# Optimization experiments

Hardware: AMD Instinct MI355X
Metric: run time of the kernel (lower is better)

Reference implementation:

```python
import jax, jax.numpy as jnp
import numpy as np

N = 20000      # nodes
E = 640000     # edges (before self-loops)
NFEAT = 512
NHID = 128
HEADS = 2
NOUT = 64
K = 100
ALPHA = 0.2          # LeakyReLU negative slope
CLUSTER_TEMP = 5.0


def gat_layer(x, W, a_src, a_dst, b, src, dst, n, heads, out_c, neg_slope):
    """PyG-style GATConv (eval mode, self-loops already in src/dst).
    W: [heads*out_c, in_c], a_src/a_dst: [heads, out_c], b: [heads*out_c]."""
    h = (x @ W.T).reshape(n, heads, out_c)               # [N,H,C]
    alpha_src = (h * a_src[None]).sum(-1)                # [N,H]
    alpha_dst = (h * a_dst[None]).sum(-1)                # [N,H]
    e = alpha_src[src] + alpha_dst[dst]                  # [E',H]
    e = jnp.where(e > 0, e, neg_slope * e)               # LeakyReLU
    # segment softmax over incoming edges of each dst node
    m = jax.ops.segment_max(e, dst, num_segments=n)
    ex = jnp.exp(e - m[dst])
    s = jax.ops.segment_sum(ex, dst, num_segments=n)
    a = ex / (s[dst] + 1e-16)                            # [E',H]
    out = jax.ops.segment_sum(h[src] * a[:, :, None], dst, num_segments=n)
    return out.reshape(n, heads * out_c) + b


def cluster_iter(data_n, mu, num_iter, cluster_temp):
    """Soft k-means on row-normalized data. data_n: [N,D], mu: [K,D]."""
    def body(mu, _):
        dist = data_n @ mu.T                              # [N,K]
        r = jax.nn.softmax(cluster_temp * dist, axis=1)
        cluster_r = r.sum(axis=0)                         # [K]
        cluster_mean = r.T @ data_n                       # [K,D]
        return cluster_mean / cluster_r[:, None], None
    mu, _ = jax.lax.scan(body, mu, None, length=num_iter)
    dist = data_n @ mu.T
    r = jax.nn.softmax(cluster_temp * dist, axis=1)
    return mu, r, dist


def setup_inputs() -> dict:
    key = jax.random.key(0)
    ks = jax.random.split(key, 12)
    x = jax.random.normal(ks[0], (N, NFEAT), dtype=jnp.float32)
    edge_index = jax.random.randint(ks[1], (2, E), 0, N, dtype=jnp.int32)
    # GATConv layer 1 params
    W1 = jax.random.normal(ks[2], (HEADS * NHID, NFEAT), dtype=jnp.float32) * 0.05
    a_src1 = jax.random.normal(ks[3], (HEADS, NHID), dtype=jnp.float32) * 0.1
    a_dst1 = jax.random.normal(ks[4], (HEADS, NHID), dtype=jnp.float32) * 0.1
    b1 = jnp.zeros((HEADS * NHID,), dtype=jnp.float32)
    # GATConv layer 2 params (heads=1)
    W2 = jax.random.normal(ks[5], (NOUT, HEADS * NHID), dtype=jnp.float32) * 0.05
    a_src2 = jax.random.normal(ks[6], (1, NOUT), dtype=jnp.float32) * 0.1
    a_dst2 = jax.random.normal(ks[7], (1, NOUT), dtype=jnp.float32) * 0.1
    b2 = jnp.zeros((NOUT,), dtype=jnp.float32)
    # cluster init (self.init = torch.rand(K, nout))
    mu0 = jax.random.uniform(ks[8], (K, NOUT), dtype=jnp.float32)
    return {"x": x, "W1": W1, "a_src1": a_src1, "a_dst1": a_dst1, "b1": b1,
            "W2": W2, "a_src2": a_src2, "a_dst2": a_dst2, "b2": b2,
            "mu0": mu0, "edge_index": edge_index, "num_iter": 10}


def reference(x, W1, a_src1, a_dst1, b1, W2, a_src2, a_dst2, b2, mu0,
              edge_index, num_iter):
    loops = jnp.arange(N, dtype=edge_index.dtype)
    src = jnp.concatenate([edge_index[0], loops])
    dst = jnp.concatenate([edge_index[1], loops])
    h = jax.nn.elu(gat_layer(x, W1, a_src1, a_dst1, b1, src, dst,
                             N, HEADS, NHID, ALPHA))
    embeds = gat_layer(h, W2, a_src2, a_dst2, b2, src, dst,
                       N, 1, NOUT, ALPHA) + 1e-6
    data_n = embeds / jnp.linalg.norm(embeds, axis=1, keepdims=True)
    mu_init, _, _ = cluster_iter(data_n, mu0, num_iter, CLUSTER_TEMP)
    mu, r, dist = cluster_iter(data_n, jax.lax.stop_gradient(mu_init), 1,
                               CLUSTER_TEMP)
    return mu, r, embeds, dist
```

## Files before the change

### kernel.cpp

```cpp
#include <hip/hip_runtime.h>
#include <math.h>

#define Nn 20000
#define Ee 640000
#define ETOT 660000
#define NF 512
#define C1 256
#define C2 64
#define KC 100
#define TEMP 5.0f
#define NSLOPE 0.2f
#define NPART 250
#define CHB 80

__device__ __forceinline__ float wredSum(float v) {
#pragma unroll
  for (int off = 32; off > 0; off >>= 1) v += __shfl_xor(v, off, 64);
  return v;
}
__device__ __forceinline__ float wredMax(float v) {
#pragma unroll
  for (int off = 32; off > 0; off >>= 1) v = fmaxf(v, __shfl_xor(v, off, 64));
  return v;
}
__device__ __forceinline__ float bredSum(float v, volatile float* red) {
  v = wredSum(v);
  __syncthreads();
  if ((threadIdx.x & 63) == 0) red[threadIdx.x >> 6] = v;
  __syncthreads();
  return red[0] + red[1] + red[2] + red[3];
}
__device__ __forceinline__ float bredMax(float v, volatile float* red) {
  v = wredMax(v);
  __syncthreads();
  if ((threadIdx.x & 63) == 0) red[threadIdx.x >> 6] = v;
  __syncthreads();
  return fmaxf(fmaxf(red[0], red[1]), fmaxf(red[2], red[3]));
}

__global__ void hist_kernel(const int* __restrict__ ei, int* __restrict__ deg) {
  int e = blockIdx.x * 256 + threadIdx.x;
  if (e >= ETOT) return;
  int dst = e < Ee ? ei[Ee + e] : e - Ee;
  atomicAdd(&deg[dst], 1);
}

__global__ __launch_bounds__(1024) void scan2_kernel(const int* __restrict__ deg,
    int* __restrict__ rowp, int* __restrict__ curs) {
  __shared__ int wsum[16];
  __shared__ int wpre[16];
  int t = threadIdx.x;
  int lane = t & 63, w = t >> 6;
  int loc[20];
  int tot = 0;
  int base = t * 20;
  if (t < 1000) {
#pragma unroll
    for (int i = 0; i < 20; i++) { tot += deg[base + i]; loc[i] = tot; }
  }
  int s = tot;
#pragma unroll
  for (int off = 1; off < 64; off <<= 1) {
    int u = __shfl_up(s, off, 64);
    if (lane >= off) s += u;
  }
  if (lane == 63) wsum[w] = s;
  __syncthreads();
  if (t == 0) {
    int c = 0;
#pragma unroll
    for (int i = 0; i < 16; i++) { c += wsum[i]; wpre[i] = c; }
    rowp[0] = 0;
  }
  __syncthreads();
  int p = (w > 0 ? wpre[w - 1] : 0) + s - tot;
  if (t < 1000) {
    int prev = 0;
#pragma unroll
    for (int i = 0; i < 20; i++) {
      rowp[base + i + 1] = p + loc[i];
      curs[base + i] = p + prev;
      prev = loc[i];
    }
  }
}

__global__ void scatter_kernel(const int* __restrict__ ei, int* __restrict__ curs,
                               int* __restrict__ esort) {
  int e = blockIdx.x * 256 + threadIdx.x;
  if (e >= ETOT) return;
  int dst = e < Ee ? ei[Ee + e] : e - Ee;
  int pos = atomicAdd(&curs[dst], 1);
  esort[pos] = e;
}

__global__ __launch_bounds__(256) void gemm128(const float* __restrict__ A,
    const float* __restrict__ B, float* __restrict__ C, int M, int N, int K) {
  __shared__ __align__(16) float As[16][132];
  __shared__ __align__(16) float Bs[16][132];
  int tid = threadIdx.x;
  int bm = blockIdx.x << 7, bn = blockIdx.y << 7;
  int tx = tid & 15, ty = tid >> 4;
  int r0 = tid >> 2;
  int c0 = (tid & 3) << 2;
  float acc[2][2][4][4] = {};
  for (int k0 = 0; k0 < K; k0 += 16) {
    float4 a0 = make_float4(0.f, 0.f, 0.f, 0.f), a1 = a0;
    int am0 = bm + r0, am1 = bm + 64 + r0;
    if (am0 < M) a0 = *(const float4*)(A + (size_t)am0 * K + k0 + c0);
    if (am1 < M) a1 = *(const float4*)(A + (size_t)am1 * K + k0 + c0);
    float4 b0 = *(const float4*)(B + (size_t)(bn + r0) * K + k0 + c0);
    float4 b1 = *(const float4*)(B + (size_t)(bn + 64 + r0) * K + k0 + c0);
    __syncthreads();
    As[c0 + 0][r0] = a0.x; As[c0 + 1][r0] = a0.y; As[c0 + 2][r0] = a0.z; As[c0 + 3][r0] = a0.w;
    As[c0 + 0][64 + r0] = a1.x; As[c0 + 1][64 + r0] = a1.y; As[c0 + 2][64 + r0] = a1.z; As[c0 + 3][64 + r0] = a1.w;
    Bs[c0 + 0][r0] = b0.x; Bs[c0 + 1][r0] = b0.y; Bs[c0 + 2][r0] = b0.z; Bs[c0 + 3][r0] = b0.w;
    Bs[c0 + 0][64 + r0] = b1.x; Bs[c0 + 1][64 + r0] = b1.y; Bs[c0 + 2][64 + r0] = b1.z; Bs[c0 + 3][64 + r0] = b1.w;
    __syncthreads();
#pragma unroll
    for (int k = 0; k < 16; k++) {
      float4 av0 = *(const float4*)&As[k][ty << 2];
      float4 av1 = *(const float4*)&As[k][64 + (ty << 2)];
      float4 bv0 = *(const float4*)&Bs[k][tx << 2];
      float4 bv1 = *(const float4*)&Bs[k][64 + (tx << 2)];
      float aa[2][4] = {{av0.x, av0.y, av0.z, av0.w}, {av1.x, av1.y, av1.z, av1.w}};
      float bb[2][4] = {{bv0.x, bv0.y, bv0.z, bv0.w}, {bv1.x, bv1.y, bv1.z, bv1.w}};
#pragma unroll
      for (int im = 0; im < 2; im++)
#pragma unroll
        for (int i = 0; i < 4; i++)
#pragma unroll
          for (int jn = 0; jn < 2; jn++)
#pragma unroll
            for (int j = 0; j < 4; j++)
              acc[im][jn][i][j] += aa[im][i] * bb[jn][j];
    }
  }
#pragma unroll
  for (int im = 0; im < 2; im++)
#pragma unroll
    for (int i = 0; i < 4; i++) {
      int row = bm + (im << 6) + (ty << 2) + i;
      if (row < M) {
#pragma unroll
        for (int jn = 0; jn < 2; jn++) {
          float4 v = make_float4(acc[im][jn][i][0], acc[im][jn][i][1],
                                 acc[im][jn][i][2], acc[im][jn][i][3]);
          *(float4*)(C + (size_t)row * N + bn + (jn << 6) + (tx << 2)) = v;
        }
      }
    }
}

__global__ __launch_bounds__(256) void gemm_nt(const float* __restrict__ A,
    const float* __restrict__ B, float* __restrict__ C, int M, int N, int K) {
  __shared__ __align__(16) float As[16][68];
  __shared__ __align__(16) float Bs[16][68];
  int tid = threadIdx.x;
  int bm = blockIdx.x << 6, bn = blockIdx.y << 6;
  int lr = tid >> 2;
  int lc = (tid & 3) << 2;
  int tx = tid & 15, ty = tid >> 4;
  float acc[4][4] = {};
  for (int k0 = 0; k0 < K; k0 += 16) {
    int am = bm + lr;
    float4 av = make_float4(0.f, 0.f, 0.f, 0.f);
    if (am < M) av = *(const float4*)(A + (size_t)am * K + k0 + lc);
    float4 bv = *(const float4*)(B + (size_t)(bn + lr) * K + k0 + lc);
    __syncthreads();
    As[lc + 0][lr] = av.x; As[lc + 1][lr] = av.y; As[lc + 2][lr] = av.z; As[lc + 3][lr] = av.w;
    Bs[lc + 0][lr] = bv.x; Bs[lc + 1][lr] = bv.y; Bs[lc + 2][lr] = bv.z; Bs[lc + 3][lr] = bv.w;
    __syncthreads();
#pragma unroll
    for (int k = 0; k < 16; k++) {
      float4 a = *(const float4*)&As[k][ty << 2];
      float4 b = *(const float4*)&Bs[k][tx << 2];
      float aa[4] = {a.x, a.y, a.z, a.w};
      float bb[4] = {b.x, b.y, b.z, b.w};
#pragma unroll
      for (int i = 0; i < 4; i++)
#pragma unroll
        for (int j = 0; j < 4; j++) acc[i][j] += aa[i] * bb[j];
    }
  }
#pragma unroll
  for (int i = 0; i < 4; i++) {
    int row = bm + (ty << 2) + i;
    if (row < M) {
#pragma unroll
      for (int j = 0; j < 4; j++)
        C[(size_t)row * N + bn + (tx << 2) + j] = acc[i][j];
    }
  }
}

__global__ __launch_bounds__(256) void alpha1_kernel(const float* __restrict__ h,
    const float* __restrict__ a_src, const float* __restrict__ a_dst,
    float* __restrict__ asn, float* __restrict__ adn) {
  int l = threadIdx.x & 63;
  int n = (blockIdx.x << 2) + (threadIdx.x >> 6);
  if (n >= Nn) return;
  const float* hr = h + (size_t)n * C1;
  float h0 = hr[l], h1v = hr[64 + l], h2v = hr[128 + l], h3v = hr[192 + l];
  float ps0 = h0 * a_src[l] + h1v * a_src[64 + l];
  float pd0 = h0 * a_dst[l] + h1v * a_dst[64 + l];
  float ps1 = h2v * a_src[128 + l] + h3v * a_src[192 + l];
  float pd1 = h2v * a_dst[128 + l] + h3v * a_dst[192 + l];
  ps0 = wredSum(ps0); pd0 = wredSum(pd0); ps1 = wredSum(ps1); pd1 = wredSum(pd1);
  if (l == 0) {
    asn[2 * n] = ps0; asn[2 * n + 1] = ps1;
    adn[2 * n] = pd0; adn[2 * n + 1] = pd1;
  }
}

__global__ __launch_bounds__(256) void alpha2_kernel(const float* __restrict__ h,
    const float* __restrict__ a_src, const float* __restrict__ a_dst,
    float* __restrict__ asn, float* __restrict__ adn) {
  int l = threadIdx.x & 63;
  int n = (blockIdx.x << 2) + (threadIdx.x >> 6);
  if (n >= Nn) return;
  float v = h[(size_t)n * C2 + l];
  float ps = wredSum(v * a_src[l]);
  float pd = wredSum(v * a_dst[l]);
  if (l == 0) { asn[n] = ps; adn[n] = pd; }
}

__global__ __launch_bounds__(256) void agg1_kernel(const float* __restrict__ h,
    const float* __restrict__ asn, const float* __restrict__ adn,
    const float* __restrict__ b1, const int* __restrict__ ei,
    const int* __restrict__ rowp, const int* __restrict__ esort,
    float* __restrict__ ho) {
  __shared__ float red[4];
  __shared__ float w0[64], w1[64];
  __shared__ int ss[64];
  int n = blockIdx.x, tid = threadIdx.x;
  int lo = rowp[n], hi = rowp[n + 1];
  float ad0 = adn[2 * n], ad1 = adn[2 * n + 1];
  float m0 = -1e30f, m1 = -1e30f;
  for (int i = lo + tid; i < hi; i += 256) {
    int eid = esort[i];
    int s = eid < Ee ? ei[eid] : eid - Ee;
    float e0 = asn[2 * s] + ad0;     e0 = e0 > 0.f ? e0 : NSLOPE * e0;
    float e1 = asn[2 * s + 1] + ad1; e1 = e1 > 0.f ? e1 : NSLOPE * e1;
    m0 = fmaxf(m0, e0); m1 = fmaxf(m1, e1);
  }
  m0 = bredMax(m0, red);
  m1 = bredMax(m1, red);
  float s0 = 0.f, s1 = 0.f;
  for (int i = lo + tid; i < hi; i += 256) {
    int eid = esort[i];
    int s = eid < Ee ? ei[eid] : eid - Ee;
    float e0 = asn[2 * s] + ad0;     e0 = e0 > 0.f ? e0 : NSLOPE * e0;
    float e1 = asn[2 * s + 1] + ad1; e1 = e1 > 0.f ? e1 : NSLOPE * e1;
    s0 += expf(e0 - m0); s1 += expf(e1 - m1);
  }
  s0 = bredSum(s0, red) + 1e-16f;
  s1 = bredSum(s1, red) + 1e-16f;
  float r0 = 1.0f / s0, r1 = 1.0f / s1;
  float acc = 0.f;
  int c = tid;
  const bool hi_head = (tid & 128) != 0;
  for (int base = lo; base < hi; base += 64) {
    int cnt = min(64, hi - base);
    __syncthreads();
    if (tid < cnt) {
      int eid = esort[base + tid];
      int s = eid < Ee ? ei[eid] : eid - Ee;
      float e0 = asn[2 * s] + ad0;     e0 = e0 > 0.f ? e0 : NSLOPE * e0;
      float e1 = asn[2 * s + 1] + ad1; e1 = e1 > 0.f ? e1 : NSLOPE * e1;
      w0[tid] = expf(e0 - m0) * r0;
      w1[tid] = expf(e1 - m1) * r1;
      ss[tid] = s;
    }
    __syncthreads();
    const float* hw = hi_head ? w1 : w0;
    for (int j = 0; j < cnt; j++)
      acc += h[(size_t)ss[j] * C1 + c] * hw[j];
  }
  float v = acc + b1[c];
  ho[(size_t)n * C1 + c] = v > 0.f ? v : expf(v) - 1.0f;
}

__global__ __launch_bounds__(64) void agg2_kernel(const float* __restrict__ h,
    const float* __restrict__ asn, const float* __restrict__ adn,
    const float* __restrict__ b2, const int* __restrict__ ei,
    const int* __restrict__ rowp, const int* __restrict__ esort,
    float* __restrict__ emb, float* __restrict__ dnrm) {
  __shared__ float wv[64];
  __shared__ int ss[64];
  int n = blockIdx.x, l = threadIdx.x;
  int lo = rowp[n], hi = rowp[n + 1];
  float ad = adn[n];
  float m = -1e30f;
  for (int i = lo + l; i < hi; i += 64) {
    int eid = esort[i];
    int s = eid < Ee ? ei[eid] : eid - Ee;
    float e = asn[s] + ad; e = e > 0.f ? e : NSLOPE * e;
    m = fmaxf(m, e);
  }
  m = wredMax(m);
  float sum = 0.f;
  for (int i = lo + l; i < hi; i += 64) {
    int eid = esort[i];
    int s = eid < Ee ? ei[eid] : eid - Ee;
    float e = asn[s] + ad; e = e > 0.f ? e : NSLOPE * e;
    sum += expf(e - m);
  }
  sum = wredSum(sum) + 1e-16f;
  float rs = 1.0f / sum;
  float acc = 0.f;
  for (int base = lo; base < hi; base += 64) {
    int cnt = min(64, hi - base);
    __syncthreads();
    if (l < cnt) {
      int eid = esort[base + l];
      int s = eid < Ee ? ei[eid] : eid - Ee;
      float e = asn[s] + ad; e = e > 0.f ? e : NSLOPE * e;
      wv[l] = expf(e - m) * rs;
      ss[l] = s;
    }
    __syncthreads();
    for (int j = 0; j < cnt; j++)
      acc += h[(size_t)ss[j] * C2 + l] * wv[j];
  }
  float e = acc + b2[l] + 1e-6f;
  float nrm = sqrtf(wredSum(e * e));
  emb[(size_t)n * C2 + l] = e;
  dnrm[(size_t)n * C2 + l] = e / nrm;
}

template <int MODE>
__global__ __launch_bounds__(256) void fused_ac(
    const float* __restrict__ dnp, const float* __restrict__ mu_init,
    const float* __restrict__ mu, float* __restrict__ pcm, float* __restrict__ pcr,
    float* __restrict__ rout, float* __restrict__ distout,
    int it, const int* __restrict__ niter) {
  if (MODE == 0) { if (it > niter[0]) return; }
  __shared__ float mu_s[KC * 65];
  __shared__ __align__(16) float d_s[CHB * 68];
  __shared__ float r_s[CHB * KC];
  int tid = threadIdx.x, blk = blockIdx.x;
  const float* msrc = (MODE == 0 && false) ? mu_init : ((MODE == 0 && it == 0) ? mu_init : mu);
  for (int idx = tid; idx < KC * 64; idx += 256)
    mu_s[(idx >> 6) * 65 + (idx & 63)] = msrc[idx];
  for (int idx = tid; idx < CHB * 64; idx += 256) {
    int row = idx >> 6, col = idx & 63;
    d_s[row * 68 + col] = dnp[(size_t)blk * (CHB * 64) + idx];
  }
  __syncthreads();
  int w = tid >> 6, l = tid & 63;
  const bool has2 = l < (KC - 64);
  int l2 = has2 ? 64 + l : l;
  for (int g = 0; g < 5; g++) {
    int nl0 = w * 20 + g * 4;
    float z1[4] = {0.f, 0.f, 0.f, 0.f}, z2[4] = {0.f, 0.f, 0.f, 0.f};
#pragma unroll 8
    for (int d = 0; d < 64; d++) {
      float m1v = mu_s[l * 65 + d];
      float m2v = mu_s[l2 * 65 + d];
#pragma unroll
      for (int nb = 0; nb < 4; nb++) {
        float dv = d_s[(nl0 + nb) * 68 + d];
        z1[nb] += m1v * dv;
        z2[nb] += m2v * dv;
      }
    }
#pragma unroll
    for (int nb = 0; nb < 4; nb++) {
      float g1 = TEMP * z1[nb];
      float g2 = has2 ? TEMP * z2[nb] : -1e30f;
      float m = wredMax(fmaxf(g1, g2));
      float e1 = expf(g1 - m);
      float e2 = has2 ? expf(g2 - m) : 0.f;
      float inv = 1.0f / wredSum(e1 + e2);
      int nl = nl0 + nb;
      if (MODE == 0) {
        r_s[nl * KC + l] = e1 * inv;
        if (has2) r_s[nl * KC + 64 + l] = e2 * inv;
      } else {
        size_t n = (size_t)blk * CHB + nl;
        rout[n * KC + l] = e1 * inv;
        if (has2) rout[n * KC + 64 + l] = e2 * inv;
        distout[n * KC + l] = z1[nb];
        if (has2) distout[n * KC + 64 + l] = z2[nb];
      }
    }
  }
  if (MODE == 0) {
    __syncthreads();
    int tx = tid & 15, ky = tid >> 4;
    float acc[7][4] = {};
    float accr[7] = {};
    for (int j = 0; j < CHB; j++) {
      float4 dv = *(const float4*)&d_s[j * 68 + (tx << 2)];
#pragma unroll
      for (int jj = 0; jj < 7; jj++) {
        int kk = ky + (jj << 4);
        if (kk < KC) {
          float rv = r_s[j * KC + kk];
          acc[jj][0] += rv * dv.x; acc[jj][1] += rv * dv.y;
          acc[jj][2] += rv * dv.z; acc[jj][3] += rv * dv.w;
          if (tx == 0) accr[jj] += rv;
        }
      }
    }
#pragma unroll
    for (int jj = 0; jj < 7; jj++) {
      int kk = ky + (jj << 4);
      if (kk < KC) {
        float* p = pcm + (size_t)blk * 6400 + kk * 64 + (tx << 2);
        p[0] = acc[jj][0]; p[1] = acc[jj][1]; p[2] = acc[jj][2]; p[3] = acc[jj][3];
        if (tx == 0) pcr[blk * KC + kk] = accr[jj];
      }
    }
  }
}

__global__ __launch_bounds__(256) void muupd_kernel(const float* __restrict__ pcm,
    const float* __restrict__ pcr, float* __restrict__ mu,
    int it, const int* __restrict__ niter) {
  if (it > niter[0]) return;
  __shared__ float part[4][64];
  __shared__ float red[4];
  int k = blockIdx.x, tid = threadIdx.x;
  int d = tid & 63, bg = tid >> 6;
  float s = 0.f;
  for (int b = bg; b < NPART; b += 4)
    s += pcm[(size_t)b * 6400 + k * 64 + d];
  part[bg][d] = s;
  float c = (tid < NPART) ? pcr[tid * KC + k] : 0.f;
  c = wredSum(c);
  if ((tid & 63) == 0) red[tid >> 6] = c;
  __syncthreads();
  if (tid < 64) {
    float cr = red[0] + red[1] + red[2] + red[3];
    mu[k * 64 + tid] = (part[0][tid] + part[1][tid] + part[2][tid] + part[3][tid]) / cr;
  }
}

__global__ void copy_f(const float* __restrict__ a, float* __restrict__ b, int n) {
  int i = blockIdx.x * 256 + threadIdx.x;
  if (i < n) b[i] = a[i];
}

extern "C" void kernel_launch(void* const* d_in, const int* in_sizes, int n_in,
                              void* d_out, int out_size, void* d_ws, size_t ws_size,
                              hipStream_t stream) {
  const float* x    = (const float*)d_in[0];
  const float* W1   = (const float*)d_in[1];
  const float* asr1 = (const float*)d_in[2];
  const float* ads1 = (const float*)d_in[3];
  const float* b1   = (const float*)d_in[4];
  const float* W2   = (const float*)d_in[5];
  const float* asr2 = (const float*)d_in[6];
  const float* ads2 = (const float*)d_in[7];
  const float* b2   = (const float*)d_in[8];
  const float* mu0  = (const float*)d_in[9];
  const int*   ei   = (const int*)d_in[10];
  const int*   nit  = (const int*)d_in[11];

  float* f = (float*)d_ws;
  float* h1   = f;  f += (size_t)Nn * C1;
  float* h1o  = f;  f += (size_t)Nn * C1;
  float* as1  = f;  f += Nn * 2;
  float* ad1  = f;  f += Nn * 2;
  float* h2   = f;  f += (size_t)Nn * C2;
  float* as2  = f;  f += Nn;
  float* ad2  = f;  f += Nn;
  float* dn   = f;  f += (size_t)Nn * C2;
  float* pcm  = f;  f += (size_t)NPART * 6400;
  float* pcr  = f;  f += NPART * KC;
  float* mu   = f;  f += KC * C2;
  int* ip = (int*)f;
  int* deg   = ip;  ip += Nn;
  int* rowp  = ip;  ip += Nn + 1;
  int* curs  = ip;  ip += Nn;
  int* esort = ip;  ip += ETOT;

  float* out_mu = (float*)d_out;
  float* out_r  = out_mu + KC * C2;
  float* out_e  = out_r + (size_t)Nn * KC;
  float* out_d  = out_e + (size_t)Nn * C2;

  hipMemsetAsync(deg, 0, Nn * sizeof(int), stream);
  hist_kernel<<<(ETOT + 255) / 256, 256, 0, stream>>>(ei, deg);
  scan2_kernel<<<1, 1024, 0, stream>>>(deg, rowp, curs);
  scatter_kernel<<<(ETOT + 255) / 256, 256, 0, stream>>>(ei, curs, esort);

  gemm128<<<dim3(157, 2), 256, 0, stream>>>(x, W1, h1, Nn, C1, NF);
  alpha1_kernel<<<5000, 256, 0, stream>>>(h1, asr1, ads1, as1, ad1);
  agg1_kernel<<<Nn, 256, 0, stream>>>(h1, as1, ad1, b1, ei, rowp, esort, h1o);

  gemm_nt<<<dim3(313, 1), 256, 0, stream>>>(h1o, W2, h2, Nn, C2, C1);
  alpha2_kernel<<<5000, 256, 0, stream>>>(h2, asr2, ads2, as2, ad2);
  agg2_kernel<<<Nn, 64, 0, stream>>>(h2, as2, ad2, b2, ei, rowp, esort, out_e, dn);

  for (int it = 0; it < 12; it++) {
    fused_ac<0><<<NPART, 256, 0, stream>>>(dn, mu0, mu, pcm, pcr, nullptr, nullptr, it, nit);
    muupd_kernel<<<KC, 256, 0, stream>>>(pcm, pcr, mu, it, nit);
  }
  fused_ac<1><<<NPART, 256, 0, stream>>>(dn, mu0, mu, nullptr, nullptr, out_r, out_d, 0, nit);
  copy_f<<<25, 256, 0, stream>>>(mu, out_mu, KC * C2);
}
```

Measured before the change: 1.173 ms.

## Precompute per-edge attention logits and restructure GAT aggregation with online softmax

The scatter step now stores the source and destination node IDs in CSR order instead of an edge-ID permutation. New edge kernels precompute the LeakyReLU attention logits per sorted edge, so aggregation no longer does the double indirection through esort and ei or recomputes logits three times. The aggregation kernels use a single-pass online softmax and gather float4 rows across warps with two accumulators. agg2 also packs four nodes per 256-thread block. The cost is extra workspace and two extra launches, plus fast __expf in place of expf.

```diff
diff --git a/kernel.cpp b/kernel.cpp
--- a/kernel.cpp
+++ b/kernel.cpp
@@ -23,20 +23,6 @@
   for (int off = 32; off > 0; off >>= 1) v = fmaxf(v, __shfl_xor(v, off, 64));
   return v;
 }
-__device__ __forceinline__ float bredSum(float v, volatile float* red) {
-  v = wredSum(v);
-  __syncthreads();
-  if ((threadIdx.x & 63) == 0) red[threadIdx.x >> 6] = v;
-  __syncthreads();
-  return red[0] + red[1] + red[2] + red[3];
-}
-__device__ __forceinline__ float bredMax(float v, volatile float* red) {
-  v = wredMax(v);
-  __syncthreads();
-  if ((threadIdx.x & 63) == 0) red[threadIdx.x >> 6] = v;
-  __syncthreads();
-  return fmaxf(fmaxf(red[0], red[1]), fmaxf(red[2], red[3]));
-}
 
 __global__ void hist_kernel(const int* __restrict__ ei, int* __restrict__ deg) {
   int e = blockIdx.x * 256 + threadIdx.x;
@@ -86,12 +72,37 @@
 }
 
 __global__ void scatter_kernel(const int* __restrict__ ei, int* __restrict__ curs,
-                               int* __restrict__ esort) {
+                               int* __restrict__ ssort, int* __restrict__ dsort) {
   int e = blockIdx.x * 256 + threadIdx.x;
   if (e >= ETOT) return;
+  int src = e < Ee ? ei[e] : e - Ee;
   int dst = e < Ee ? ei[Ee + e] : e - Ee;
   int pos = atomicAdd(&curs[dst], 1);
-  esort[pos] = e;
+  ssort[pos] = src;
+  dsort[pos] = dst;
+}
+
+__global__ __launch_bounds__(256) void edge_e1(const int* __restrict__ ssort,
+    const int* __restrict__ dsort, const float* __restrict__ asn,
+    const float* __restrict__ adn, float2* __restrict__ eb) {
+  int i = blockIdx.x * 256 + threadIdx.x;
+  if (i >= ETOT) return;
+  int s = ssort[i], d = dsort[i];
+  float2 a = ((const float2*)asn)[s];
+  float2 b = ((const float2*)adn)[d];
+  float e0 = a.x + b.x, e1 = a.y + b.y;
+  e0 = e0 > 0.f ? e0 : NSLOPE * e0;
+  e1 = e1 > 0.f ? e1 : NSLOPE * e1;
+  eb[i] = make_float2(e0, e1);
+}
+
+__global__ __launch_bounds__(256) void edge_e2(const int* __restrict__ ssort,
+    const int* __restrict__ dsort, const float* __restrict__ asn,
+    const float* __restrict__ adn, float* __restrict__ eb) {
+  int i = blockIdx.x * 256 + threadIdx.x;
+  if (i >= ETOT) return;
+  float e = asn[ssort[i]] + adn[dsort[i]];
+  eb[i] = e > 0.f ? e : NSLOPE * e;
 }
 
 __global__ __launch_bounds__(256) void gemm128(const float* __restrict__ A,
@@ -226,107 +237,140 @@
 }
 
 __global__ __launch_bounds__(256) void agg1_kernel(const float* __restrict__ h,
-    const float* __restrict__ asn, const float* __restrict__ adn,
-    const float* __restrict__ b1, const int* __restrict__ ei,
-    const int* __restrict__ rowp, const int* __restrict__ esort,
+    const float2* __restrict__ eb, const int* __restrict__ ssort,
+    const float* __restrict__ b1, const int* __restrict__ rowp,
     float* __restrict__ ho) {
-  __shared__ float red[4];
-  __shared__ float w0[64], w1[64];
-  __shared__ int ss[64];
+  __shared__ float redm[8], reds[8];
+  __shared__ __align__(16) float slab[4][256];
   int n = blockIdx.x, tid = threadIdx.x;
+  int w = tid >> 6, l = tid & 63;
   int lo = rowp[n], hi = rowp[n + 1];
-  float ad0 = adn[2 * n], ad1 = adn[2 * n + 1];
-  float m0 = -1e30f, m1 = -1e30f;
+  float m0 = -1e30f, s0 = 0.f, m1 = -1e30f, s1 = 0.f;
   for (int i = lo + tid; i < hi; i += 256) {
-    int eid = esort[i];
-    int s = eid < Ee ? ei[eid] : eid - Ee;
-    float e0 = asn[2 * s] + ad0;     e0 = e0 > 0.f ? e0 : NSLOPE * e0;
-    float e1 = asn[2 * s + 1] + ad1; e1 = e1 > 0.f ? e1 : NSLOPE * e1;
-    m0 = fmaxf(m0, e0); m1 = fmaxf(m1, e1);
-  }
-  m0 = bredMax(m0, red);
-  m1 = bredMax(m1, red);
-  float s0 = 0.f, s1 = 0.f;
-  for (int i = lo + tid; i < hi; i += 256) {
-    int eid = esort[i];
-    int s = eid < Ee ? ei[eid] : eid - Ee;
-    float e0 = asn[2 * s] + ad0;     e0 = e0 > 0.f ? e0 : NSLOPE * e0;
-    float e1 = asn[2 * s + 1] + ad1; e1 = e1 > 0.f ? e1 : NSLOPE * e1;
-    s0 += expf(e0 - m0); s1 += expf(e1 - m1);
-  }
-  s0 = bredSum(s0, red) + 1e-16f;
-  s1 = bredSum(s1, red) + 1e-16f;
-  float r0 = 1.0f / s0, r1 = 1.0f / s1;
-  float acc = 0.f;
-  int c = tid;
-  const bool hi_head = (tid & 128) != 0;
-  for (int base = lo; base < hi; base += 64) {
-    int cnt = min(64, hi - base);
-    __syncthreads();
-    if (tid < cnt) {
-      int eid = esort[base + tid];
-      int s = eid < Ee ? ei[eid] : eid - Ee;
-      float e0 = asn[2 * s] + ad0;     e0 = e0 > 0.f ? e0 : NSLOPE * e0;
-      float e1 = asn[2 * s + 1] + ad1; e1 = e1 > 0.f ? e1 : NSLOPE * e1;
-      w0[tid] = expf(e0 - m0) * r0;
-      w1[tid] = expf(e1 - m1) * r1;
-      ss[tid] = s;
-    }
-    __syncthreads();
-    const float* hw = hi_head ? w1 : w0;
-    for (int j = 0; j < cnt; j++)
-      acc += h[(size_t)ss[j] * C1 + c] * hw[j];
-  }
-  float v = acc + b1[c];
-  ho[(size_t)n * C1 + c] = v > 0.f ? v : expf(v) - 1.0f;
-}
-
-__global__ __launch_bounds__(64) void agg2_kernel(const float* __restrict__ h,
-    const float* __restrict__ asn, const float* __restrict__ adn,
-    const float* __restrict__ b2, const int* __restrict__ ei,
-    const int* __restrict__ rowp, const int* __restrict__ esort,
+    float2 e = eb[i];
+    if (e.x > m0) { s0 = s0 * __expf(m0 - e.x) + 1.f; m0 = e.x; }
+    else s0 += __expf(e.x - m0);
+    if (e.y > m1) { s1 = s1 * __expf(m1 - e.y) + 1.f; m1 = e.y; }
+    else s1 += __expf(e.y - m1);
+  }
+#pragma unroll
+  for (int off = 32; off > 0; off >>= 1) {
+    float om = __shfl_xor(m0, off, 64), os = __shfl_xor(s0, off, 64);
+    float nm = fmaxf(m0, om);
+    s0 = s0 * __expf(m0 - nm) + os * __expf(om - nm); m0 = nm;
+    om = __shfl_xor(m1, off, 64); os = __shfl_xor(s1, off, 64);
+    nm = fmaxf(m1, om);
+    s1 = s1 * __expf(m1 - nm) + os * __expf(om - nm); m1 = nm;
+  }
+  if (l == 0) { redm[w] = m0; reds[w] = s0; redm[4 + w] = m1; reds[4 + w] = s1; }
+  __syncthreads();
+  float M0 = fmaxf(fmaxf(redm[0], redm[1]), fmaxf(redm[2], redm[3]));
+  float M1 = fmaxf(fmaxf(redm[4], redm[5]), fmaxf(redm[6], redm[7]));
+  float S0 = reds[0] * __expf(redm[0] - M0) + reds[1] * __expf(redm[1] - M0)
+           + reds[2] * __expf(redm[2] - M0) + reds[3] * __expf(redm[3] - M0);
+  float S1 = reds[4] * __expf(redm[4] - M1) + reds[5] * __expf(redm[5] - M1)
+           + reds[6] * __expf(redm[6] - M1) + reds[7] * __expf(redm[7] - M1);
+  float inv0 = 1.f / (S0 + 1e-16f), inv1 = 1.f / (S1 + 1e-16f);
+  const bool lo_head = (l < 32);
+  float Msel = lo_head ? M0 : M1;
+  float isel = lo_head ? inv0 : inv1;
+  int ch = l << 2;
+  int deg = hi - lo;
+  float4 accA = {0.f, 0.f, 0.f, 0.f}, accB = {0.f, 0.f, 0.f, 0.f};
+  int j = w;
+  for (; j + 4 < deg; j += 8) {
+    int i0 = lo + j, i1 = lo + j + 4;
+    float2 eA = eb[i0];
+    float2 eB = eb[i1];
+    int sA = ssort[i0], sB = ssort[i1];
+    float4 ha = *(const float4*)(h + (size_t)sA * C1 + ch);
+    float4 hb = *(const float4*)(h + (size_t)sB * C1 + ch);
+    float wtA = __expf((lo_head ? eA.x : eA.y) - Msel) * isel;
+    float wtB = __expf((lo_head ? eB.x : eB.y) - Msel) * isel;
+    accA.x += wtA * ha.x; accA.y += wtA * ha.y; accA.z += wtA * ha.z; accA.w += wtA * ha.w;
+    accB.x += wtB * hb.x; accB.y += wtB * hb.y; accB.z += wtB * hb.z; accB.w += wtB * hb.w;
+  }
+  if (j < deg) {
+    int i0 = lo + j;
+    float2 eA = eb[i0];
+    int sA = ssort[i0];
+    float4 ha = *(const float4*)(h + (size_t)sA * C1 + ch);
+    float wtA = __expf((lo_head ? eA.x : eA.y) - Msel) * isel;
+    accA.x += wtA * ha.x; accA.y += wtA * ha.y; accA.z += wtA * ha.z; accA.w += wtA * ha.w;
+  }
+  accA.x += accB.x; accA.y += accB.y; accA.z += accB.z; accA.w += accB.w;
+  *(float4*)&slab[w][ch] = accA;
+  __syncthreads();
+  float v = slab[0][tid] + slab[1][tid] + slab[2][tid] + slab[3][tid] + b1[tid];
+  ho[(size_t)n * C1 + tid] = v > 0.f ? v : __expf(v) - 1.0f;
+}
+
+__global__ __launch_bounds__(256) void agg2_kernel(const float* __restrict__ h,
+    const float* __restrict__ eb, const int* __restrict__ ssort,
+    const float* __restrict__ b2, const int* __restrict__ rowp,
     float* __restrict__ emb, float* __restrict__ dnrm) {
-  __shared__ float wv[64];
-  __shared__ int ss[64];
-  int n = blockIdx.x, l = threadIdx.x;
+  int tid = threadIdx.x;
+  int w = tid >> 6, l = tid & 63;
+  int n = (blockIdx.x << 2) + w;
   int lo = rowp[n], hi = rowp[n + 1];
-  float ad = adn[n];
-  float m = -1e30f;
+  float m = -1e30f, s = 0.f;
   for (int i = lo + l; i < hi; i += 64) {
-    int eid = esort[i];
-    int s = eid < Ee ? ei[eid] : eid - Ee;
-    float e = asn[s] + ad; e = e > 0.f ? e : NSLOPE * e;
-    m = fmaxf(m, e);
-  }
-  m = wredMax(m);
-  float sum = 0.f;
-  for (int i = lo + l; i < hi; i += 64) {
-    int eid = esort[i];
-    int s = eid < Ee ? ei[eid] : eid - Ee;
-    float e = asn[s] + ad; e = e > 0.f ? e : NSLOPE * e;
-    sum += expf(e - m);
-  }
-  sum = wredSum(sum) + 1e-16f;
-  float rs = 1.0f / sum;
-  float acc = 0.f;
-  for (int base = lo; base < hi; base += 64) {
-    int cnt = min(64, hi - base);
-    __syncthreads();
-    if (l < cnt) {
-      int eid = esort[base + l];
-      int s = eid < Ee ? ei[eid] : eid - Ee;
-      float e = asn[s] + ad; e = e > 0.f ? e : NSLOPE * e;
-      wv[l] = expf(e - m) * rs;
-      ss[l] = s;
-    }
-    __syncthreads();
-    for (int j = 0; j < cnt; j++)
-      acc += h[(size_t)ss[j] * C2 + l] * wv[j];
-  }
-  float e = acc + b2[l] + 1e-6f;
-  float nrm = sqrtf(wredSum(e * e));
-  emb[(size_t)n * C2 + l] = e;
-  dnrm[(size_t)n * C2 + l] = e / nrm;
+    float e = eb[i];
+    if (e > m) { s = s * __expf(m - e) + 1.f; m = e; }
+    else s += __expf(e - m);
+  }
+#pragma unroll
+  for (int off = 32; off > 0; off >>= 1) {
+    float om = __shfl_xor(m, off, 64), os = __shfl_xor(s, off, 64);
+    float nm = fmaxf(m, om);
+    s = s * __expf(m - nm) + os * __expf(om - nm); m = nm;
+  }
+  float inv = 1.f / (s + 1e-16f);
+  int g = l >> 4, lg = l & 15, ch = lg << 2;
+  int deg = hi - lo;
+  float4 accA = {0.f, 0.f, 0.f, 0.f}, accB = {0.f, 0.f, 0.f, 0.f};
+  int j = g;
+  for (; j + 4 < deg; j += 8) {
+    int i0 = lo + j, i1 = lo + j + 4;
+    float eA = eb[i0], eB = eb[i1];
+    int sA = ssort[i0], sB = ssort[i1];
+    float4 ha = *(const float4*)(h + (size_t)sA * C2 + ch);
+    float4 hb = *(const float4*)(h + (size_t)sB * C2 + ch);
+    float wtA = __expf(eA - m) * inv;
+    float wtB = __expf(eB - m) * inv;
+    accA.x += wtA * ha.x; accA.y += wtA * ha.y; accA.z += wtA * ha.z; accA.w += wtA * ha.w;
+    accB.x += wtB * hb.x; accB.y += wtB * hb.y; accB.z += wtB * hb.z; accB.w += wtB * hb.w;
+  }
+  if (j < deg) {
+    int i0 = lo + j;
+    float eA = eb[i0];
+    int sA = ssort[i0];
+    float4 ha = *(const float4*)(h + (size_t)sA * C2 + ch);
+    float wtA = __expf(eA - m) * inv;
+    accA.x += wtA * ha.x; accA.y += wtA * ha.y; accA.z += wtA * ha.z; accA.w += wtA * ha.w;
+  }
+  accA.x += accB.x; accA.y += accB.y; accA.z += accB.z; accA.w += accB.w;
+#pragma unroll
+  for (int off = 16; off <= 32; off <<= 1) {
+    accA.x += __shfl_xor(accA.x, off, 64);
+    accA.y += __shfl_xor(accA.y, off, 64);
+    accA.z += __shfl_xor(accA.z, off, 64);
+    accA.w += __shfl_xor(accA.w, off, 64);
+  }
+  float4 bv = *(const float4*)(b2 + ch);
+  float e0 = accA.x + bv.x + 1e-6f;
+  float e1 = accA.y + bv.y + 1e-6f;
+  float e2 = accA.z + bv.z + 1e-6f;
+  float e3 = accA.w + bv.w + 1e-6f;
+  float dot = e0 * e0 + e1 * e1 + e2 * e2 + e3 * e3;
+#pragma unroll
+  for (int off = 1; off < 16; off <<= 1) dot += __shfl_xor(dot, off, 64);
+  float invn = 1.f / sqrtf(dot);
+  if (g == 0) {
+    *(float4*)(emb + (size_t)n * C2 + ch) = make_float4(e0, e1, e2, e3);
+    *(float4*)(dnrm + (size_t)n * C2 + ch) =
+        make_float4(e0 * invn, e1 * invn, e2 * invn, e3 * invn);
+  }
 }
 
 template <int MODE>
@@ -340,7 +384,7 @@
   __shared__ __align__(16) float d_s[CHB * 68];
   __shared__ float r_s[CHB * KC];
   int tid = threadIdx.x, blk = blockIdx.x;
-  const float* msrc = (MODE == 0 && false) ? mu_init : ((MODE == 0 && it == 0) ? mu_init : mu);
+  const float* msrc = (MODE == 0 && it == 0) ? mu_init : mu;
   for (int idx = tid; idx < KC * 64; idx += 256)
     mu_s[(idx >> 6) * 65 + (idx & 63)] = msrc[idx];
   for (int idx = tid; idx < CHB * 64; idx += 256) {
@@ -471,11 +515,14 @@
   float* pcm  = f;  f += (size_t)NPART * 6400;
   float* pcr  = f;  f += NPART * KC;
   float* mu   = f;  f += KC * C2;
+  float2* ebA = (float2*)f; f += (size_t)ETOT * 2;
+  float* ebB  = (float*)ebA;
   int* ip = (int*)f;
   int* deg   = ip;  ip += Nn;
   int* rowp  = ip;  ip += Nn + 1;
   int* curs  = ip;  ip += Nn;
-  int* esort = ip;  ip += ETOT;
+  int* ssort = ip;  ip += ETOT;
+  int* dsort = ip;  ip += ETOT;
 
   float* out_mu = (float*)d_out;
   float* out_r  = out_mu + KC * C2;
@@ -485,15 +532,17 @@
   hipMemsetAsync(deg, 0, Nn * sizeof(int), stream);
   hist_kernel<<<(ETOT + 255) / 256, 256, 0, stream>>>(ei, deg);
   scan2_kernel<<<1, 1024, 0, stream>>>(deg, rowp, curs);
-  scatter_kernel<<<(ETOT + 255) / 256, 256, 0, stream>>>(ei, curs, esort);
+  scatter_kernel<<<(ETOT + 255) / 256, 256, 0, stream>>>(ei, curs, ssort, dsort);
 
   gemm128<<<dim3(157, 2), 256, 0, stream>>>(x, W1, h1, Nn, C1, NF);
   alpha1_kernel<<<5000, 256, 0, stream>>>(h1, asr1, ads1, as1, ad1);
-  agg1_kernel<<<Nn, 256, 0, stream>>>(h1, as1, ad1, b1, ei, rowp, esort, h1o);
+  edge_e1<<<(ETOT + 255) / 256, 256, 0, stream>>>(ssort, dsort, as1, ad1, ebA);
+  agg1_kernel<<<Nn, 256, 0, stream>>>(h1, ebA, ssort, b1, rowp, h1o);
 
   gemm_nt<<<dim3(313, 1), 256, 0, stream>>>(h1o, W2, h2, Nn, C2, C1);
   alpha2_kernel<<<5000, 256, 0, stream>>>(h2, asr2, ads2, as2, ad2);
-  agg2_kernel<<<Nn, 64, 0, stream>>>(h2, as2, ad2, b2, ei, rowp, esort, out_e, dn);
+  edge_e2<<<(ETOT + 255) / 256, 256, 0, stream>>>(ssort, dsort, as2, ad2, ebB);
+  agg2_kernel<<<5000, 256, 0, stream>>>(h2, ebB, ssort, b2, rowp, out_e, dn);
 
   for (int it = 0; it < 12; it++) {
     fused_ac<0><<<NPART, 256, 0, stream>>>(dn, mu0, mu, pcm, pcr, nullptr, nullptr, it, nit);
```

Result: faster. 1.146 ms (-2.3%).
